# Performance work log

Hardware: AMD Instinct MI355X
Metric: run time of the kernel (lower is better)

Reference implementation:

```python
import jax, jax.numpy as jnp
import numpy as np

B, H, W, C = 32, 56, 56, 192
HEADS = 6
WS = 7            # window size
SS = 3            # shift size
N = WS * WS       # tokens per window (49)
HID = 4 * C
EPS = 1e-5


def _rel_index():
    coords = np.stack(np.meshgrid(np.arange(WS), np.arange(WS), indexing='ij')).reshape(2, -1)
    rel = (coords[:, :, None] - coords[:, None, :]).transpose(1, 2, 0)
    rel[:, :, 0] += WS - 1
    rel[:, :, 1] += WS - 1
    rel[:, :, 0] *= 2 * WS - 1
    return rel.sum(-1)  # [N, N] int


def _attn_mask():
    # shift mask, identical to the torch construction; static -> numpy
    m = np.zeros((H, W))
    cnt = 0
    for hs in (slice(0, -WS), slice(-WS, -SS), slice(-SS, None)):
        for ws in (slice(0, -WS), slice(-WS, -SS), slice(-SS, None)):
            m[hs, ws] = cnt
            cnt += 1
    mw = m.reshape(H // WS, WS, W // WS, WS).transpose(0, 2, 1, 3).reshape(-1, N)  # [nW, N]
    diff = mw[:, None, :] - mw[:, :, None]
    return np.where(diff != 0, -100.0, 0.0).astype(np.float32)  # [nW, N, N]

REL_IDX = jnp.asarray(_rel_index())
ATTN_MASK = jnp.asarray(_attn_mask())


def setup_inputs() -> dict:
    key = jax.random.key(0)
    ks = jax.random.split(key, 16)
    s = 0.02
    return {
        'x': jax.random.normal(ks[0], (B, H, W, C), jnp.float32),
        'norm1_g': jnp.ones((C,), jnp.float32),
        'norm1_b': jnp.zeros((C,), jnp.float32),
        'qkv_w': jax.random.normal(ks[1], (C, 3 * C), jnp.float32) * s,
        'qkv_b': jnp.zeros((3 * C,), jnp.float32),
        'proj_w': jax.random.normal(ks[2], (C, C), jnp.float32) * s,
        'proj_b': jnp.zeros((C,), jnp.float32),
        'bias_table': jax.random.normal(ks[3], ((2 * WS - 1) ** 2, HEADS), jnp.float32) * s,
        'norm2_g': jnp.ones((C,), jnp.float32),
        'norm2_b': jnp.zeros((C,), jnp.float32),
        'fc1_w': jax.random.normal(ks[4], (C, HID), jnp.float32) * s,
        'fc1_b': jnp.zeros((HID,), jnp.float32),
        'fc2_w': jax.random.normal(ks[5], (HID, C), jnp.float32) * s,
        'fc2_b': jnp.zeros((C,), jnp.float32),
    }


def _ln(x, g, b):
    mu = jnp.mean(x, -1, keepdims=True)
    var = jnp.var(x, -1, keepdims=True)
    return (x - mu) * jax.lax.rsqrt(var + EPS) * g + b


def _partition(x):
    # [B,H,W,C] -> [B*nW, N, C]
    return x.reshape(B, H // WS, WS, W // WS, WS, C).transpose(0, 1, 3, 2, 4, 5).reshape(-1, N, C)


def _reverse(w):
    # [B*nW, N, C] -> [B,H,W,C]
    return w.reshape(B, H // WS, W // WS, WS, WS, C).transpose(0, 1, 3, 2, 4, 5).reshape(B, H, W, C)


def reference(x, norm1_g, norm1_b, qkv_w, qkv_b, proj_w, proj_b, bias_table,
              norm2_g, norm2_b, fc1_w, fc1_b, fc2_w, fc2_b):
    hd = C // HEADS
    scale = hd ** -0.5
    sc = x
    h = _ln(x, norm1_g, norm1_b)
    h = jnp.roll(h, (-SS, -SS), (1, 2))
    xw = _partition(h)                                  # [B_, N, C]
    B_ = xw.shape[0]
    qkv = (xw @ qkv_w + qkv_b).reshape(B_, N, 3, HEADS, hd).transpose(2, 0, 3, 1, 4)
    q, k, v = qkv[0], qkv[1], qkv[2]                    # [B_, H, N, hd]
    attn = jnp.einsum('bhnd,bhmd->bhnm', q * scale, k)  # [B_, H, N, N]
    bias = bias_table[REL_IDX.reshape(-1)].reshape(N, N, HEADS).transpose(2, 0, 1)
    attn = attn + bias[None]
    nW = (H // WS) * (W // WS)
    attn = attn.reshape(B, nW, HEADS, N, N) + ATTN_MASK[None, :, None]
    attn = jax.nn.softmax(attn.reshape(-1, HEADS, N, N), axis=-1)
    out = jnp.einsum('bhnm,bhmd->bhnd', attn, v).transpose(0, 2, 1, 3).reshape(B_, N, C)
    out = out @ proj_w + proj_b
    h = _reverse(out)
    h = jnp.roll(h, (SS, SS), (1, 2))
    y = sc + h
    m = _ln(y, norm2_g, norm2_b)
    mlp = jax.nn.gelu(m @ fc1_w + fc1_b, approximate=False) @ fc2_w + fc2_b
    return y + mlp
```

## Files before the change

### kernel.cpp

```cpp
#include <hip/hip_runtime.h>
#include <hip/hip_bf16.h>

typedef __hip_bfloat16 bf16;
typedef float f32x4 __attribute__((ext_vector_type(4)));
typedef short bf16x8 __attribute__((ext_vector_type(8)));
typedef short short4v __attribute__((ext_vector_type(4)));
typedef unsigned int u32;

#define NTOK 100352
#define CC 192
#define HIDN 768

__device__ __forceinline__ float b2f(unsigned short u) {
    union { unsigned int u32v; float f; } x; x.u32v = ((unsigned int)u) << 16; return x.f;
}
__device__ __forceinline__ unsigned short f2b(float f) {
    union { float f; unsigned int u; } x; x.f = f;
    unsigned int r = x.u + 0x7FFF + ((x.u >> 16) & 1);
    return (unsigned short)(r >> 16);
}
__device__ __forceinline__ float gelu_f(float x) {
    return x / (1.0f + __expf(-1.702f * x));
}

typedef __attribute__((address_space(1))) const unsigned char gas_u8;
typedef __attribute__((address_space(3))) unsigned char las_u8;
__device__ __forceinline__ void gload_lds16(const void* g, void* l) {
    __builtin_amdgcn_global_load_lds((gas_u8*)g, (las_u8*)l, 16, 0, 0);
}

__global__ void transpose_k(const float* __restrict__ src, bf16* __restrict__ dst, int R, int C) {
    int idx = blockIdx.x * 256 + threadIdx.x;
    if (idx >= R * C) return;
    int r = idx / C, c = idx % C;
    dst[(size_t)c * R + r] = __float2bfloat16(src[idx]);
}

__global__ void bm_k(const float* __restrict__ btab, float* __restrict__ bm) {
    int idx = blockIdx.x * 256 + threadIdx.x;
    if (idx >= 98304) return;
    int reg = idx & 3, lane = (idx >> 2) & 63, tile = (idx >> 8) & 15;
    int rest = idx >> 12, h = rest % 6, cls = rest / 6;
    int mt = tile >> 2, nt = tile & 3;
    int kk = mt * 16 + (lane >> 4) * 4 + reg;
    int q  = nt * 16 + (lane & 15);
    float v;
    if (kk >= 49 || q >= 49) v = -1e9f;
    else {
        int i1 = q / 7, j1 = q % 7, i2 = kk / 7, j2 = kk % 7;
        v = btab[((i1 - i2 + 6) * 13 + (j1 - j2 + 6)) * 6 + h];
        int hb7 = cls >> 1, wb7 = cls & 1;
        int r1 = (hb7 ? (i1 < 4 ? 1 : 2) : 0) * 3 + (wb7 ? (j1 < 4 ? 1 : 2) : 0);
        int r2 = (hb7 ? (i2 < 4 ? 1 : 2) : 0) * 3 + (wb7 ? (j2 < 4 ? 1 : 2) : 0);
        if (r1 != r2) v -= 100.0f;
    }
    bm[idx] = v;
}

template<bool GATHER>
__global__ __launch_bounds__(256) void ln_k(const float* __restrict__ src,
                                            const float* __restrict__ gamma,
                                            const float* __restrict__ beta,
                                            bf16* __restrict__ dst) {
    int wave = threadIdx.x >> 6, lane = threadIdx.x & 63;
    int t = blockIdx.x * 4 + wave;
    size_t srow;
    if (GATHER) {
        int w = t / 49, n = t % 49;
        int b = w >> 6, wl = w & 63, hb = wl >> 3, wb = wl & 7;
        int i = n / 7, j = n % 7;
        int sh = hb * 7 + i + 3; if (sh >= 56) sh -= 56;
        int sw = wb * 7 + j + 3; if (sw >= 56) sw -= 56;
        srow = ((size_t)(b * 56 + sh) * 56 + sw) * CC;
    } else {
        srow = (size_t)t * CC;
    }
    float v[4];
    int c = lane * 4;
    float sum = 0.f, sq = 0.f;
    if (lane < 48) {
        f32x4 d = *(const f32x4*)(src + srow + c);
        #pragma unroll
        for (int q = 0; q < 4; ++q) { v[q] = d[q]; sum += v[q]; sq += v[q] * v[q]; }
    }
    #pragma unroll
    for (int off = 1; off < 64; off <<= 1) { sum += __shfl_xor(sum, off); sq += __shfl_xor(sq, off); }
    float mu = sum * (1.0f / 192.0f);
    float var = sq * (1.0f / 192.0f) - mu * mu;
    float rstd = rsqrtf(var + 1e-5f);
    if (lane < 48) {
        f32x4 gg = *(const f32x4*)(gamma + c);
        f32x4 bb = *(const f32x4*)(beta + c);
        short4v o;
        #pragma unroll
        for (int q = 0; q < 4; ++q) {
            float val = (v[q] - mu) * rstd * gg[q] + bb[q];
            o[q] = (short)f2b(val);
        }
        *(short4v*)(dst + (size_t)t * CC + c) = o;
    }
}

template<int EPI>
__global__ __launch_bounds__(512) void gemm_t(
    const bf16* __restrict__ X, const bf16* __restrict__ WT,
    const float* __restrict__ bias, int K, int N,
    bf16* __restrict__ outb, float* __restrict__ outf,
    const float* __restrict__ xres, const float* __restrict__ yin)
{
    __shared__ bf16 As[2][256 * 64];
    __shared__ bf16 Bs[2][64 * 64];
    const int tid = threadIdx.x;
    const int w = tid >> 6, lane = tid & 63;
    const int w0 = w & 1, w1 = w >> 1;

    const u32 nwg = gridDim.x * gridDim.y;
    u32 bid = blockIdx.y * gridDim.x + blockIdx.x;
    bid = (bid & 7) * (nwg >> 3) + (bid >> 3);
    const int tn0 = (bid % gridDim.x) * 64;
    const int tm0 = (bid / gridDim.x) * 256;

    const int r16 = lane & 15, g8 = (lane >> 4) * 8;

    const bf16* gA[4];
    const bf16* gB;
    #pragma unroll
    for (int j = 0; j < 4; ++j) {
        int c = (w * 4 + j) * 64 + lane;
        int l = c ^ ((c >> 3) & 7);
        gA[j] = X + (size_t)(tm0 + (c >> 3)) * K + (l & 7) * 8;
    }
    {
        int c = w * 64 + lane;
        int l = c ^ ((c >> 3) & 7);
        gB = WT + (size_t)(tn0 + (c >> 3)) * K + (l & 7) * 8;
    }

    auto stage = [&](int buf, int kk) {
        #pragma unroll
        for (int j = 0; j < 4; ++j)
            gload_lds16(gA[j] + kk, (char*)&As[buf][0] + (size_t)(w * 4 + j) * 1024);
        gload_lds16(gB + kk, (char*)&Bs[buf][0] + (size_t)w * 1024);
    };

    f32x4 acc[4][2] = {};
    const int nt = K >> 6;
    stage(0, 0);
    __syncthreads();
    for (int t = 0; t < nt; ++t) {
        int buf = t & 1;
        if (t + 1 < nt) stage(buf ^ 1, (t + 1) << 6);
        const char* ab = (const char*)&As[buf][0];
        const char* bb_ = (const char*)&Bs[buf][0];
        #pragma unroll
        for (int k32 = 0; k32 < 2; ++k32) {
            int kcolb = k32 * 64 + g8 * 2;
            bf16x8 a[4], b[2];
            #pragma unroll
            for (int m = 0; m < 4; ++m) {
                int row = w1 * 64 + m * 16 + r16;
                int byte = row * 128 + kcolb;
                a[m] = *(const bf16x8*)(ab + (byte ^ ((row & 7) << 4)));
            }
            #pragma unroll
            for (int n = 0; n < 2; ++n) {
                int row = w0 * 32 + n * 16 + r16;
                int byte = row * 128 + kcolb;
                b[n] = *(const bf16x8*)(bb_ + (byte ^ ((row & 7) << 4)));
            }
            #pragma unroll
            for (int m = 0; m < 4; ++m)
                #pragma unroll
                for (int n = 0; n < 2; ++n)
                    acc[m][n] = __builtin_amdgcn_mfma_f32_16x16x32_bf16(a[m], b[n], acc[m][n], 0, 0, 0);
        }
        __syncthreads();
    }

    #pragma unroll
    for (int n = 0; n < 2; ++n) {
        int col = tn0 + w0 * 32 + n * 16 + r16;
        float bv = bias[col];
        #pragma unroll
        for (int m = 0; m < 4; ++m) {
            #pragma unroll
            for (int r = 0; r < 4; ++r) {
                int mm = tm0 + w1 * 64 + m * 16 + (lane >> 4) * 4 + r;
                float val = acc[m][n][r] + bv;
                if (EPI == 0) {
                    outb[(size_t)mm * N + col] = __float2bfloat16(val);
                } else if (EPI == 1) {
                    int ww = mm / 49, nn = mm % 49;
                    int b_ = ww >> 6, wl = ww & 63, hb = wl >> 3, wb = wl & 7;
                    int i = nn / 7, j = nn % 7;
                    int oh = hb * 7 + i + 3; if (oh >= 56) oh -= 56;
                    int ow = wb * 7 + j + 3; if (ow >= 56) ow -= 56;
                    size_t dst = ((size_t)(b_ * 56 + oh) * 56 + ow) * CC + col;
                    outf[dst] = xres[dst] + val;
                } else if (EPI == 2) {
                    outb[(size_t)mm * N + col] = __float2bfloat16(gelu_f(val));
                } else if (EPI == 3) {
                    outf[(size_t)mm * N + col] = val + yin[(size_t)mm * N + col];
                } else {
                    outb[((size_t)(col >> 5) * NTOK + mm) * 32 + (col & 31)] = __float2bfloat16(val);
                }
            }
        }
    }
}

__global__ __launch_bounds__(384) void attn_m(const bf16* __restrict__ qkv,
                                              const float* __restrict__ bm,
                                              bf16* __restrict__ out)
{
    __shared__ char Pl[6][8192];
    __shared__ char Vt[6][4096];
    const int w = blockIdx.x;
    const int h = threadIdx.x >> 6, l = threadIdx.x & 63;
    const int w49 = w * 49;
    const int wl = w & 63;
    const int cls = (((wl >> 3) == 7) ? 2 : 0) + (((wl & 7) == 7) ? 1 : 0);
    const int hi8 = (l >> 4) * 8, lo = l & 15;

    {
        const bf16* vbase = qkv + ((size_t)(12 + h) * NTOK + w49) * 32;
        #pragma unroll
        for (int it = 0; it < 4; ++it) {
            int c = it * 64 + l;
            int kk = c >> 2, off = (c & 3) * 8;
            bf16x8 v = {};
            if (c < 196) v = *(const bf16x8*)(vbase + kk * 32 + off);
            #pragma unroll
            for (int j = 0; j < 8; ++j) {
                int d = off + j;
                int byte = (d * 128 + kk * 2) ^ ((d & 7) << 4);
                *(bf16*)(&Vt[h][0] + byte) = ((const bf16*)&v)[j];
            }
        }
    }

    const bf16* qb = qkv + ((size_t)h * NTOK + w49) * 32 + hi8;
    const bf16* kb = qkv + ((size_t)(6 + h) * NTOK + w49) * 32 + hi8;
    bf16x8 af[4], bf_[4];
    #pragma unroll
    for (int mt = 0; mt < 4; ++mt) af[mt] = *(const bf16x8*)(kb + (size_t)(mt * 16 + lo) * 32);
    #pragma unroll
    for (int ntt = 0; ntt < 4; ++ntt) bf_[ntt] = *(const bf16x8*)(qb + (size_t)(ntt * 16 + lo) * 32);
    f32x4 acc[4][4] = {};
    #pragma unroll
    for (int mt = 0; mt < 4; ++mt)
        #pragma unroll
        for (int ntt = 0; ntt < 4; ++ntt)
            acc[mt][ntt] = __builtin_amdgcn_mfma_f32_16x16x32_bf16(af[mt], bf_[ntt], acc[mt][ntt], 0, 0, 0);

    const float scale = 0.17677669529663689f;
    const float* bmb = bm + ((size_t)(cls * 6 + h) << 4) * 256;
    #pragma unroll
    for (int mt = 0; mt < 4; ++mt)
        #pragma unroll
        for (int ntt = 0; ntt < 4; ++ntt) {
            f32x4 bmv = *(const f32x4*)(bmb + (mt * 4 + ntt) * 256 + l * 4);
            #pragma unroll
            for (int r = 0; r < 4; ++r) acc[mt][ntt][r] = acc[mt][ntt][r] * scale + bmv[r];
        }

    float inv[4], mx[4];
    #pragma unroll
    for (int ntt = 0; ntt < 4; ++ntt) {
        float m_ = -1e30f;
        #pragma unroll
        for (int mt = 0; mt < 4; ++mt)
            #pragma unroll
            for (int r = 0; r < 4; ++r) m_ = fmaxf(m_, acc[mt][ntt][r]);
        m_ = fmaxf(m_, __shfl_xor(m_, 16));
        m_ = fmaxf(m_, __shfl_xor(m_, 32));
        mx[ntt] = m_;
    }
    #pragma unroll
    for (int ntt = 0; ntt < 4; ++ntt) {
        float s_ = 0.f;
        #pragma unroll
        for (int mt = 0; mt < 4; ++mt)
            #pragma unroll
            for (int r = 0; r < 4; ++r) {
                float e = __expf(acc[mt][ntt][r] - mx[ntt]);
                acc[mt][ntt][r] = e;
                s_ += e;
            }
        s_ += __shfl_xor(s_, 16);
        s_ += __shfl_xor(s_, 32);
        inv[ntt] = 1.0f / s_;
    }

    #pragma unroll
    for (int mt = 0; mt < 4; ++mt)
        #pragma unroll
        for (int ntt = 0; ntt < 4; ++ntt)
            #pragma unroll
            for (int rp = 0; rp < 4; rp += 2) {
                u32 pk = (u32)f2b(acc[mt][ntt][rp]) | ((u32)f2b(acc[mt][ntt][rp + 1]) << 16);
                int kk = mt * 16 + (l >> 4) * 4 + rp;
                int q  = ntt * 16 + lo;
                int byte = (q * 128 + kk * 2) ^ ((q & 7) << 4);
                *(u32*)(&Pl[h][0] + byte) = pk;
            }

    f32x4 o[4][2] = {};
    #pragma unroll
    for (int ks = 0; ks < 2; ++ks) {
        int kb_ = (ks * 32 + hi8) * 2;
        bf16x8 pa[4], vb[2];
        #pragma unroll
        for (int qt = 0; qt < 4; ++qt) {
            int row = qt * 16 + lo;
            pa[qt] = *(const bf16x8*)(&Pl[h][0] + ((row * 128 + kb_) ^ ((row & 7) << 4)));
        }
        #pragma unroll
        for (int dt = 0; dt < 2; ++dt) {
            int row = dt * 16 + lo;
            vb[dt] = *(const bf16x8*)(&Vt[h][0] + ((row * 128 + kb_) ^ ((row & 7) << 4)));
        }
        #pragma unroll
        for (int qt = 0; qt < 4; ++qt)
            #pragma unroll
            for (int dt = 0; dt < 2; ++dt)
                o[qt][dt] = __builtin_amdgcn_mfma_f32_16x16x32_bf16(pa[qt], vb[dt], o[qt][dt], 0, 0, 0);
    }

    #pragma unroll
    for (int qt = 0; qt < 4; ++qt)
        #pragma unroll
        for (int r = 0; r < 4; ++r) {
            int qrow = (l >> 4) * 4 + r;
            float iv = __shfl(inv[qt], qrow);
            int q = qt * 16 + qrow;
            if (q < 49) {
                size_t ob = (size_t)(w49 + q) * CC + h * 32 + lo;
                out[ob]      = __float2bfloat16(o[qt][0][r] * iv);
                out[ob + 16] = __float2bfloat16(o[qt][1][r] * iv);
            }
        }
}

extern "C" void kernel_launch(void* const* d_in, const int* in_sizes, int n_in,
                              void* d_out, int out_size, void* d_ws, size_t ws_size,
                              hipStream_t stream) {
    const float* x      = (const float*)d_in[0];
    const float* n1g    = (const float*)d_in[1];
    const float* n1b    = (const float*)d_in[2];
    const float* qkv_w  = (const float*)d_in[3];
    const float* qkv_b  = (const float*)d_in[4];
    const float* proj_w = (const float*)d_in[5];
    const float* proj_b = (const float*)d_in[6];
    const float* btab   = (const float*)d_in[7];
    const float* n2g    = (const float*)d_in[8];
    const float* n2b    = (const float*)d_in[9];
    const float* fc1_w  = (const float*)d_in[10];
    const float* fc1_b  = (const float*)d_in[11];
    const float* fc2_w  = (const float*)d_in[12];
    const float* fc2_b  = (const float*)d_in[13];

    char* ws = (char*)d_ws;
    const size_t XW_OFF  = 0;
    const size_t QKV_OFF = 38535168;
    const size_t ATT_OFF = 154140672;
    const size_t WT_OFF  = 192675840;
    const size_t BM_OFF  = 193560576;
    if (ws_size < 193953792ull) return;

    bf16* xw   = (bf16*)(ws + XW_OFF);
    bf16* mbuf = (bf16*)(ws + XW_OFF);
    bf16* qkvb = (bf16*)(ws + QKV_OFF);
    bf16* attb = (bf16*)(ws + ATT_OFF);
    bf16* hidb = (bf16*)(ws + QKV_OFF);
    float* yf  = (float*)d_out;
    bf16* wt   = (bf16*)(ws + WT_OFF);
    float* bmt = (float*)(ws + BM_OFF);
    bf16* qkv_wT  = wt;
    bf16* proj_wT = wt + 110592;
    bf16* fc1_wT  = wt + 147456;
    bf16* fc2_wT  = wt + 294912;

    transpose_k<<<dim3(432), 256, 0, stream>>>(qkv_w, qkv_wT, 192, 576);
    transpose_k<<<dim3(144), 256, 0, stream>>>(proj_w, proj_wT, 192, 192);
    transpose_k<<<dim3(576), 256, 0, stream>>>(fc1_w, fc1_wT, 192, 768);
    transpose_k<<<dim3(576), 256, 0, stream>>>(fc2_w, fc2_wT, 768, 192);
    bm_k<<<dim3(384), 256, 0, stream>>>(btab, bmt);

    ln_k<true><<<NTOK / 4, 256, 0, stream>>>(x, n1g, n1b, xw);

    gemm_t<4><<<dim3(9, 392), 512, 0, stream>>>(
        xw, qkv_wT, qkv_b, 192, 576, qkvb, nullptr, nullptr, nullptr);
    attn_m<<<dim3(2048), 384, 0, stream>>>(qkvb, bmt, attb);
    gemm_t<1><<<dim3(3, 392), 512, 0, stream>>>(
        attb, proj_wT, proj_b, 192, 192, nullptr, yf, x, nullptr);

    ln_k<false><<<NTOK / 4, 256, 0, stream>>>(yf, n2g, n2b, mbuf);

    gemm_t<2><<<dim3(12, 392), 512, 0, stream>>>(
        mbuf, fc1_wT, fc1_b, 192, 768, hidb, nullptr, nullptr, nullptr);
    gemm_t<3><<<dim3(3, 392), 512, 0, stream>>>(
        hidb, fc2_wT, fc2_b, 768, 192, nullptr, yf, nullptr, yf);
}
```

Baseline: 391.4 us.

## Fuse output projection into attention kernel and store residual as bf16

The proj GEMM and residual add move into the attention kernel. Each block stages its normalized attention output in shared memory and multiplies it by the projection weights held in registers, then writes the shifted residual sum as bf16. This removes one GEMM launch and the round trip of the attention output buffer, and halves the traffic of the intermediate y. The weight transposes and bias-mask build are merged into a single prep kernel. Storing y in bf16 costs precision in the final residual.

```diff
diff --git a/kernel.cpp b/kernel.cpp
--- a/kernel.cpp
+++ b/kernel.cpp
@@ -29,36 +29,49 @@
     __builtin_amdgcn_global_load_lds((gas_u8*)g, (las_u8*)l, 16, 0, 0);
 }
 
-__global__ void transpose_k(const float* __restrict__ src, bf16* __restrict__ dst, int R, int C) {
+__global__ void prep_k(const float* __restrict__ qkv_w, const float* __restrict__ proj_w,
+                       const float* __restrict__ fc1_w, const float* __restrict__ fc2_w,
+                       const float* __restrict__ btab,
+                       bf16* __restrict__ qkvT, bf16* __restrict__ projT,
+                       bf16* __restrict__ fc1T, bf16* __restrict__ fc2T,
+                       float* __restrict__ bm)
+{
     int idx = blockIdx.x * 256 + threadIdx.x;
-    if (idx >= R * C) return;
-    int r = idx / C, c = idx % C;
-    dst[(size_t)c * R + r] = __float2bfloat16(src[idx]);
-}
-
-__global__ void bm_k(const float* __restrict__ btab, float* __restrict__ bm) {
-    int idx = blockIdx.x * 256 + threadIdx.x;
-    if (idx >= 98304) return;
-    int reg = idx & 3, lane = (idx >> 2) & 63, tile = (idx >> 8) & 15;
-    int rest = idx >> 12, h = rest % 6, cls = rest / 6;
-    int mt = tile >> 2, nt = tile & 3;
-    int kk = mt * 16 + (lane >> 4) * 4 + reg;
-    int q  = nt * 16 + (lane & 15);
-    float v;
-    if (kk >= 49 || q >= 49) v = -1e9f;
-    else {
-        int i1 = q / 7, j1 = q % 7, i2 = kk / 7, j2 = kk % 7;
-        v = btab[((i1 - i2 + 6) * 13 + (j1 - j2 + 6)) * 6 + h];
-        int hb7 = cls >> 1, wb7 = cls & 1;
-        int r1 = (hb7 ? (i1 < 4 ? 1 : 2) : 0) * 3 + (wb7 ? (j1 < 4 ? 1 : 2) : 0);
-        int r2 = (hb7 ? (i2 < 4 ? 1 : 2) : 0) * 3 + (wb7 ? (j2 < 4 ? 1 : 2) : 0);
-        if (r1 != r2) v -= 100.0f;
-    }
-    bm[idx] = v;
-}
-
-template<bool GATHER>
-__global__ __launch_bounds__(256) void ln_k(const float* __restrict__ src,
+    if (idx < 110592) {
+        int c = idx / 192, r = idx % 192;
+        qkvT[idx] = __float2bfloat16(qkv_w[(size_t)r * 576 + c]);
+    } else if (idx < 147456) {
+        int t = idx - 110592, c = t / 192, r = t % 192;
+        projT[t] = __float2bfloat16(proj_w[(size_t)r * 192 + c]);
+    } else if (idx < 294912) {
+        int t = idx - 147456, c = t / 192, r = t % 192;
+        fc1T[t] = __float2bfloat16(fc1_w[(size_t)r * 768 + c]);
+    } else if (idx < 442368) {
+        int t = idx - 294912, c = t / 768, r = t % 768;
+        fc2T[t] = __float2bfloat16(fc2_w[(size_t)r * 192 + c]);
+    } else if (idx < 540672) {
+        int t = idx - 442368;
+        int reg = t & 3, lane = (t >> 2) & 63, tile = (t >> 8) & 15;
+        int rest = t >> 12, h = rest % 6, cls = rest / 6;
+        int mt = tile >> 2, nt = tile & 3;
+        int kk = mt * 16 + (lane >> 4) * 4 + reg;
+        int q  = nt * 16 + (lane & 15);
+        float v;
+        if (kk >= 49 || q >= 49) v = -1e9f;
+        else {
+            int i1 = q / 7, j1 = q % 7, i2 = kk / 7, j2 = kk % 7;
+            v = btab[((i1 - i2 + 6) * 13 + (j1 - j2 + 6)) * 6 + h];
+            int hb7 = cls >> 1, wb7 = cls & 1;
+            int r1 = (hb7 ? (i1 < 4 ? 1 : 2) : 0) * 3 + (wb7 ? (j1 < 4 ? 1 : 2) : 0);
+            int r2 = (hb7 ? (i2 < 4 ? 1 : 2) : 0) * 3 + (wb7 ? (j2 < 4 ? 1 : 2) : 0);
+            if (r1 != r2) v -= 100.0f;
+        }
+        bm[t] = v;
+    }
+}
+
+template<typename ST, bool GATHER>
+__global__ __launch_bounds__(256) void ln_k(const ST* __restrict__ src,
                                             const float* __restrict__ gamma,
                                             const float* __restrict__ beta,
                                             bf16* __restrict__ dst) {
@@ -79,9 +92,17 @@
     int c = lane * 4;
     float sum = 0.f, sq = 0.f;
     if (lane < 48) {
-        f32x4 d = *(const f32x4*)(src + srow + c);
-        #pragma unroll
-        for (int q = 0; q < 4; ++q) { v[q] = d[q]; sum += v[q]; sq += v[q] * v[q]; }
+        if constexpr (sizeof(ST) == 2) {
+            short4v d = *(const short4v*)((const bf16*)src + srow + c);
+            #pragma unroll
+            for (int q = 0; q < 4; ++q) v[q] = b2f((unsigned short)d[q]);
+        } else {
+            f32x4 d = *(const f32x4*)((const float*)src + srow + c);
+            #pragma unroll
+            for (int q = 0; q < 4; ++q) v[q] = d[q];
+        }
+        #pragma unroll
+        for (int q = 0; q < 4; ++q) { sum += v[q]; sq += v[q] * v[q]; }
     }
     #pragma unroll
     for (int off = 1; off < 64; off <<= 1) { sum += __shfl_xor(sum, off); sq += __shfl_xor(sq, off); }
@@ -106,7 +127,7 @@
     const bf16* __restrict__ X, const bf16* __restrict__ WT,
     const float* __restrict__ bias, int K, int N,
     bf16* __restrict__ outb, float* __restrict__ outf,
-    const float* __restrict__ xres, const float* __restrict__ yin)
+    const bf16* __restrict__ yin)
 {
     __shared__ bf16 As[2][256 * 64];
     __shared__ bf16 Bs[2][64 * 64];
@@ -187,20 +208,10 @@
             for (int r = 0; r < 4; ++r) {
                 int mm = tm0 + w1 * 64 + m * 16 + (lane >> 4) * 4 + r;
                 float val = acc[m][n][r] + bv;
-                if (EPI == 0) {
-                    outb[(size_t)mm * N + col] = __float2bfloat16(val);
-                } else if (EPI == 1) {
-                    int ww = mm / 49, nn = mm % 49;
-                    int b_ = ww >> 6, wl = ww & 63, hb = wl >> 3, wb = wl & 7;
-                    int i = nn / 7, j = nn % 7;
-                    int oh = hb * 7 + i + 3; if (oh >= 56) oh -= 56;
-                    int ow = wb * 7 + j + 3; if (ow >= 56) ow -= 56;
-                    size_t dst = ((size_t)(b_ * 56 + oh) * 56 + ow) * CC + col;
-                    outf[dst] = xres[dst] + val;
-                } else if (EPI == 2) {
+                if (EPI == 2) {
                     outb[(size_t)mm * N + col] = __float2bfloat16(gelu_f(val));
                 } else if (EPI == 3) {
-                    outf[(size_t)mm * N + col] = val + yin[(size_t)mm * N + col];
+                    outf[(size_t)mm * N + col] = val + __bfloat162float(yin[(size_t)mm * N + col]);
                 } else {
                     outb[((size_t)(col >> 5) * NTOK + mm) * 32 + (col & 31)] = __float2bfloat16(val);
                 }
@@ -209,12 +220,16 @@
     }
 }
 
-__global__ __launch_bounds__(384) void attn_m(const bf16* __restrict__ qkv,
-                                              const float* __restrict__ bm,
-                                              bf16* __restrict__ out)
+__global__ __launch_bounds__(384) void attn_mp(const bf16* __restrict__ qkv,
+                                               const float* __restrict__ bm,
+                                               const bf16* __restrict__ pwt,
+                                               const float* __restrict__ pbias,
+                                               const float* __restrict__ x,
+                                               bf16* __restrict__ ybf)
 {
     __shared__ char Pl[6][8192];
     __shared__ char Vt[6][4096];
+    char* At = &Pl[0][0];
     const int w = blockIdx.x;
     const int h = threadIdx.x >> 6, l = threadIdx.x & 63;
     const int w49 = w * 49;
@@ -327,6 +342,7 @@
                 o[qt][dt] = __builtin_amdgcn_mfma_f32_16x16x32_bf16(pa[qt], vb[dt], o[qt][dt], 0, 0, 0);
     }
 
+    __syncthreads();
     #pragma unroll
     for (int qt = 0; qt < 4; ++qt)
         #pragma unroll
@@ -334,12 +350,60 @@
             int qrow = (l >> 4) * 4 + r;
             float iv = __shfl(inv[qt], qrow);
             int q = qt * 16 + qrow;
+            #pragma unroll
+            for (int dt = 0; dt < 2; ++dt) {
+                int d = h * 32 + dt * 16 + lo;
+                int byte = q * 512 + ((d * 2) ^ ((q & 7) << 4));
+                *(bf16*)(At + byte) = __float2bfloat16(o[qt][dt][r] * iv);
+            }
+        }
+    bf16x8 wp[6][2];
+    {
+        const bf16* wb0 = pwt + (size_t)(h * 32 + lo) * 192 + hi8;
+        const bf16* wb1 = wb0 + (size_t)16 * 192;
+        #pragma unroll
+        for (int t6 = 0; t6 < 6; ++t6) {
+            wp[t6][0] = *(const bf16x8*)(wb0 + t6 * 32);
+            wp[t6][1] = *(const bf16x8*)(wb1 + t6 * 32);
+        }
+    }
+    float pb0 = pbias[h * 32 + lo], pb1 = pbias[h * 32 + 16 + lo];
+    __syncthreads();
+
+    f32x4 acc2[4][2] = {};
+    #pragma unroll
+    for (int t6 = 0; t6 < 6; ++t6) {
+        int k2b = (t6 * 32 + hi8) * 2;
+        bf16x8 am[4];
+        #pragma unroll
+        for (int mt = 0; mt < 4; ++mt) {
+            int q = mt * 16 + lo;
+            am[mt] = *(const bf16x8*)(At + q * 512 + (k2b ^ ((q & 7) << 4)));
+        }
+        #pragma unroll
+        for (int mt = 0; mt < 4; ++mt)
+            #pragma unroll
+            for (int nf = 0; nf < 2; ++nf)
+                acc2[mt][nf] = __builtin_amdgcn_mfma_f32_16x16x32_bf16(am[mt], wp[t6][nf], acc2[mt][nf], 0, 0, 0);
+    }
+
+    const int b_ = w >> 6, hb = wl >> 3, wb2 = wl & 7;
+    #pragma unroll
+    for (int mt = 0; mt < 4; ++mt) {
+        #pragma unroll
+        for (int r = 0; r < 4; ++r) {
+            int q = mt * 16 + (l >> 4) * 4 + r;
             if (q < 49) {
-                size_t ob = (size_t)(w49 + q) * CC + h * 32 + lo;
-                out[ob]      = __float2bfloat16(o[qt][0][r] * iv);
-                out[ob + 16] = __float2bfloat16(o[qt][1][r] * iv);
-            }
-        }
+                int i = q / 7, j = q % 7;
+                int oh = hb * 7 + i + 3; if (oh >= 56) oh -= 56;
+                int ow = wb2 * 7 + j + 3; if (ow >= 56) ow -= 56;
+                size_t dst = ((size_t)(b_ * 56 + oh) * 56 + ow) * CC;
+                int n0 = h * 32 + lo;
+                ybf[dst + n0]      = __float2bfloat16(x[dst + n0]      + acc2[mt][0][r] + pb0);
+                ybf[dst + n0 + 16] = __float2bfloat16(x[dst + n0 + 16] + acc2[mt][1][r] + pb1);
+            }
+        }
+    }
 }
 
 extern "C" void kernel_launch(void* const* d_in, const int* in_sizes, int n_in,
@@ -363,17 +427,17 @@
     char* ws = (char*)d_ws;
     const size_t XW_OFF  = 0;
     const size_t QKV_OFF = 38535168;
-    const size_t ATT_OFF = 154140672;
-    const size_t WT_OFF  = 192675840;
-    const size_t BM_OFF  = 193560576;
-    if (ws_size < 193953792ull) return;
+    const size_t YB_OFF  = 192675840;
+    const size_t WT_OFF  = 231211008;
+    const size_t BM_OFF  = 232095744;
+    if (ws_size < 232488960ull) return;
 
     bf16* xw   = (bf16*)(ws + XW_OFF);
     bf16* mbuf = (bf16*)(ws + XW_OFF);
     bf16* qkvb = (bf16*)(ws + QKV_OFF);
-    bf16* attb = (bf16*)(ws + ATT_OFF);
     bf16* hidb = (bf16*)(ws + QKV_OFF);
-    float* yf  = (float*)d_out;
+    bf16* ybf  = (bf16*)(ws + YB_OFF);
+    float* yout = (float*)d_out;
     bf16* wt   = (bf16*)(ws + WT_OFF);
     float* bmt = (float*)(ws + BM_OFF);
     bf16* qkv_wT  = wt;
@@ -381,24 +445,20 @@
     bf16* fc1_wT  = wt + 147456;
     bf16* fc2_wT  = wt + 294912;
 
-    transpose_k<<<dim3(432), 256, 0, stream>>>(qkv_w, qkv_wT, 192, 576);
-    transpose_k<<<dim3(144), 256, 0, stream>>>(proj_w, proj_wT, 192, 192);
-    transpose_k<<<dim3(576), 256, 0, stream>>>(fc1_w, fc1_wT, 192, 768);
-    transpose_k<<<dim3(576), 256, 0, stream>>>(fc2_w, fc2_wT, 768, 192);
-    bm_k<<<dim3(384), 256, 0, stream>>>(btab, bmt);
-
-    ln_k<true><<<NTOK / 4, 256, 0, stream>>>(x, n1g, n1b, xw);
+    prep_k<<<dim3(2112), 256, 0, stream>>>(qkv_w, proj_w, fc1_w, fc2_w, btab,
+                                           qkv_wT, proj_wT, fc1_wT, fc2_wT, bmt);
+
+    ln_k<float, true><<<NTOK / 4, 256, 0, stream>>>(x, n1g, n1b, xw);
 
     gemm_t<4><<<dim3(9, 392), 512, 0, stream>>>(
-        xw, qkv_wT, qkv_b, 192, 576, qkvb, nullptr, nullptr, nullptr);
-    attn_m<<<dim3(2048), 384, 0, stream>>>(qkvb, bmt, attb);
-    gemm_t<1><<<dim3(3, 392), 512, 0, stream>>>(
-        attb, proj_wT, proj_b, 192, 192, nullptr, yf, x, nullptr);
-
-    ln_k<false><<<NTOK / 4, 256, 0, stream>>>(yf, n2g, n2b, mbuf);
+        xw, qkv_wT, qkv_b, 192, 576, qkvb, nullptr, nullptr);
+
+    attn_mp<<<dim3(2048), 384, 0, stream>>>(qkvb, bmt, proj_wT, proj_b, x, ybf);
+
+    ln_k<bf16, false><<<NTOK / 4, 256, 0, stream>>>(ybf, n2g, n2b, mbuf);
 
     gemm_t<2><<<dim3(12, 392), 512, 0, stream>>>(
-        mbuf, fc1_wT, fc1_b, 192, 768, hidb, nullptr, nullptr, nullptr);
+        mbuf, fc1_wT, fc1_b, 192, 768, hidb, nullptr, nullptr);
     gemm_t<3><<<dim3(3, 392), 512, 0, stream>>>(
-        hidb, fc2_wT, fc2_b, 768, 192, nullptr, yf, nullptr, yf);
-}
+        hidb, fc2_wT, fc2_b, 768, 192, nullptr, yout, ybf);
+}
```

Result: faster. 343.6 us (-12.2%).
